# Optimization experiments

Hardware: AMD Instinct MI355X
Metric: run time of the kernel (lower is better)

## Reference

```python
import jax, jax.numpy as jnp
import numpy as np

NUM_HEADS = 8
AGENT_NUM = 144
POOL_SIZE = 12  # int(sqrt(agent_num))


def _adaptive_pool_matrix(H, out):
    # Row i averages input rows [floor(i*H/out), ceil((i+1)*H/out)) -- PyTorch AdaptiveAvgPool2d semantics.
    P = np.zeros((out, H), dtype=np.float32)
    for i in range(out):
        s = (i * H) // out
        e = -((-(i + 1) * H) // out)
        P[i, s:e] = 1.0 / (e - s)
    return jnp.asarray(P)


def setup_inputs() -> dict:
    key = jax.random.key(0)
    ks = jax.random.split(key, 4)
    b, n, c = 16, 3136, 512
    return {
        "x": jax.random.normal(ks[0], (b, n, c), dtype=jnp.float32),
        "qkv_w": jax.random.normal(ks[1], (3 * c, c), dtype=jnp.float32) * 0.02,
        "proj_w": jax.random.normal(ks[2], (c, c), dtype=jnp.float32) * 0.02,
        "proj_b": jnp.zeros((c,), dtype=jnp.float32),
        "dwc_w": jax.random.normal(ks[3], (c, 1, 3, 3), dtype=jnp.float32) * 0.1,
        "dwc_b": jnp.zeros((c,), dtype=jnp.float32),
    }


def reference(x, qkv_w, proj_w, proj_b, dwc_w, dwc_b):
    b, n, c = x.shape
    H = NUM_HEADS
    d = c // H
    hh = int(n ** 0.5)  # 56
    scale = d ** -0.5

    qkv = x @ qkv_w.T  # (b, n, 3c)
    q, k, v = jnp.split(qkv, 3, axis=-1)

    # adaptive avg pool of q (as b,h,w,c image) down to 12x12 -> agent tokens
    P = _adaptive_pool_matrix(hh, POOL_SIZE)  # (12, 56)
    agent = jnp.einsum('ph,qw,bhwc->bpqc', P, P, q.reshape(b, hh, hh, c))
    agent = agent.reshape(b, AGENT_NUM, c)

    def heads(t):
        return t.reshape(b, -1, H, d).transpose(0, 2, 1, 3)  # (b, H, L, d)

    qh, kh, vh, ah = heads(q), heads(k), heads(v), heads(agent)

    # stage 1: agent-to-key attention
    agent_attn = jax.nn.softmax((ah * scale) @ kh.transpose(0, 1, 3, 2), axis=-1)  # (b,H,144,n)
    agent_v = agent_attn @ vh  # (b,H,144,d)

    # stage 2: query-to-agent attention
    q_attn = jax.nn.softmax((qh * scale) @ ah.transpose(0, 1, 3, 2), axis=-1)  # (b,H,n,144)
    out = (q_attn @ agent_v).transpose(0, 2, 1, 3).reshape(b, n, c)

    # depthwise 3x3 conv residual on v image
    v_img = v.reshape(b, hh, hh, c).transpose(0, 3, 1, 2)  # NCHW
    dw = jax.lax.conv_general_dilated(
        v_img, dwc_w, window_strides=(1, 1), padding='SAME',
        feature_group_count=c, dimension_numbers=('NCHW', 'OIHW', 'NCHW'))
    dw = dw + dwc_b[None, :, None, None]
    out = out + dw.transpose(0, 2, 3, 1).reshape(b, n, c)

    return out @ proj_w.T + proj_b
```

## Files before the change

### kernel.cpp

```cpp
#include <hip/hip_runtime.h>
#include <hip/hip_bf16.h>
#include <math.h>

typedef unsigned short u16;
typedef __attribute__((ext_vector_type(8))) unsigned short u16x8;
typedef __attribute__((ext_vector_type(8))) short bf16x8;
typedef __attribute__((ext_vector_type(4))) float f32x4;

#define BATCH 16
#define NTOK  3136
#define CHN   512
#define NH    8
#define HD    64
#define HHW   56
#define NAG   144
#define PS    12

#define S1PP   72
#define S2PP   152
#define ASP    72
#define AVP    152
#define TRP    136

__device__ __forceinline__ float b2f(u16 u) {
    unsigned int x = ((unsigned int)u) << 16;
    float f;
    __builtin_memcpy(&f, &x, 4);
    return f;
}
__device__ __forceinline__ u16 f2b(float f) {
    unsigned int x;
    __builtin_memcpy(&x, &f, 4);
    unsigned int lsb = (x >> 16) & 1u;
    x += 0x7fffu + lsb;
    return (u16)(x >> 16);
}
__device__ __forceinline__ void store1(float* p, float v) { *p = v; }
__device__ __forceinline__ void store1(u16* p, float v)   { *p = f2b(v); }

__global__ __launch_bounds__(256) void cvt_f32_bf16_kernel(
    const float* __restrict__ src, u16* __restrict__ dst, int n4)
{
    const int idx = blockIdx.x * 256 + threadIdx.x;
    if (idx >= n4) return;
    float4 v = reinterpret_cast<const float4*>(src)[idx];
    ushort4 o;
    o.x = f2b(v.x); o.y = f2b(v.y); o.z = f2b(v.z); o.w = f2b(v.w);
    reinterpret_cast<ushort4*>(dst)[idx] = o;
}

template <typename OT, bool BIAS, bool TRB>
__global__ __launch_bounds__(256) void mfma_gemm_kernel(
    const u16* __restrict__ A, const u16* __restrict__ W,
    const float* __restrict__ bias, OT* __restrict__ out,
    u16* __restrict__ vt_out)
{
    __shared__ u16 SH[TRB ? 128 * TRP : 16384];
    u16* Asm = SH;
    u16* Bsm = SH + 8192;

    const int tid  = threadIdx.x;
    const int lane = tid & 63;
    const int w    = tid >> 6;

    const int nwg = gridDim.x * gridDim.y;
    const int lid = blockIdx.y * gridDim.x + blockIdx.x;
    int wid = lid;
    if ((nwg & 7) == 0) {
        const int chunk = nwg >> 3;
        wid = (lid & 7) * chunk + (lid >> 3);
    }
    const int m0 = (wid >> 2) * 128;
    const int n0 = (wid & 3) * 128;

    const int wm   = (w & 1) * 64;
    const int wn   = (w >> 1) * 64;

    const int srow = lane >> 3;
    const int scol = (lane & 7) * 8;

    f32x4 acc[4][4] = {};

    for (int kt = 0; kt < 8; ++kt) {
        const int k0 = kt * 64;
        __syncthreads();
        #pragma unroll
        for (int i = 0; i < 4; ++i) {
            const int rb = w * 8 + i * 32;
            __builtin_amdgcn_global_load_lds(
                (const __attribute__((address_space(1))) void*)
                    (A + (size_t)(m0 + rb + srow) * 512 + k0 + scol),
                (__attribute__((address_space(3))) void*)(Asm + rb * 64),
                16, 0, 0);
        }
        #pragma unroll
        for (int i = 0; i < 4; ++i) {
            const int rb = w * 8 + i * 32;
            __builtin_amdgcn_global_load_lds(
                (const __attribute__((address_space(1))) void*)
                    (W + (size_t)(n0 + rb + srow) * 512 + k0 + scol),
                (__attribute__((address_space(3))) void*)(Bsm + rb * 64),
                16, 0, 0);
        }
        __syncthreads();

        #pragma unroll
        for (int kh = 0; kh < 2; ++kh) {
            bf16x8 af[4], bfr[4];
            #pragma unroll
            for (int t = 0; t < 4; ++t)
                af[t] = *reinterpret_cast<const bf16x8*>(
                    &Asm[(wm + t * 16 + (lane & 15)) * 64 + kh * 32 + (lane >> 4) * 8]);
            #pragma unroll
            for (int t = 0; t < 4; ++t)
                bfr[t] = *reinterpret_cast<const bf16x8*>(
                    &Bsm[(wn + t * 16 + (lane & 15)) * 64 + kh * 32 + (lane >> 4) * 8]);
            #pragma unroll
            for (int i = 0; i < 4; ++i)
                #pragma unroll
                for (int j = 0; j < 4; ++j)
                    acc[i][j] = __builtin_amdgcn_mfma_f32_16x16x32_bf16(
                        af[i], bfr[j], acc[i][j], 0, 0, 0);
        }
    }

    const int quad = lane >> 4;
    const int col  = lane & 15;
    #pragma unroll
    for (int j = 0; j < 4; ++j) {
        const int n = n0 + wn + j * 16 + col;
        const float bv = BIAS ? bias[n] : 0.f;
        #pragma unroll
        for (int i = 0; i < 4; ++i) {
            #pragma unroll
            for (int r = 0; r < 4; ++r) {
                const int m = m0 + wm + i * 16 + quad * 4 + r;
                store1(&out[(size_t)m * 512 + n], acc[i][j][r] + bv);
            }
        }
    }

    if constexpr (TRB) {
        __syncthreads();
        #pragma unroll
        for (int j = 0; j < 4; ++j) {
            const int nl = wn + j * 16 + col;
            #pragma unroll
            for (int i = 0; i < 4; ++i)
                #pragma unroll
                for (int r = 0; r < 4; ++r) {
                    const int ml = wm + i * 16 + quad * 4 + r;
                    SH[nl * TRP + ml] = f2b(acc[i][j][r]);
                }
        }
        __syncthreads();
        const int nr = tid >> 1, mh = (tid & 1) * 64;
        const int ng = n0 + nr;
        #pragma unroll
        for (int kc = 0; kc < 8; ++kc) {
            const int ml  = mh + kc * 8;
            const int gm  = m0 + ml;
            const int bb  = gm / NTOK;
            const int tok = gm - bb * NTOK;
            u16x8 val = *reinterpret_cast<const u16x8*>(&SH[nr * TRP + ml]);
            *reinterpret_cast<u16x8*>(
                &vt_out[((size_t)bb * CHN + ng) * NTOK + tok]) = val;
        }
    }
}

__global__ __launch_bounds__(256) void pool_x_kernel(
    const float* __restrict__ x, u16* __restrict__ x_pool)
{
    const int b = blockIdx.x, pq = blockIdx.y;
    const int p = pq / PS, qq = pq % PS;
    const int sp_ = (p * HHW) / PS, ep_ = ((p + 1) * HHW + PS - 1) / PS;
    const int sq_ = (qq * HHW) / PS, eq_ = ((qq + 1) * HHW + PS - 1) / PS;
    const float inv = 1.0f / (float)((ep_ - sp_) * (eq_ - sq_));
    for (int ch = threadIdx.x; ch < CHN; ch += 256) {
        float acc = 0.f;
        for (int y = sp_; y < ep_; ++y)
            for (int xx = sq_; xx < eq_; ++xx)
                acc += x[((size_t)b * NTOK + y * HHW + xx) * CHN + ch];
        x_pool[((size_t)b * NAG + pq) * CHN + ch] = f2b(acc * inv);
    }
}

__global__ __launch_bounds__(64) void stage1_mfma_kernel(
    const u16* __restrict__ k, const u16* __restrict__ vt,
    const u16* __restrict__ agent, u16* __restrict__ avt)
{
    __shared__ u16 Pl[16 * S1PP];

    const int lb   = blockIdx.x;
    const int work = (lb & 7) * 144 + (lb >> 3);
    const int at   = work % 9;
    const int r2   = work / 9;
    const int h    = r2 & 7;
    const int b    = r2 >> 3;

    const int lane = threadIdx.x;
    const int c = lane & 15, g = lane >> 4;

    const u16* kp = k  + (size_t)b * NTOK * CHN + h * HD;
    const u16* vp = vt + ((size_t)(b * NH + h)) * HD * NTOK;
    const u16* ap = agent + ((size_t)b * NAG + at * 16 + c) * CHN + h * HD + g * 8;

    bf16x8 af0 = *reinterpret_cast<const bf16x8*>(ap);
    bf16x8 af1 = *reinterpret_cast<const bf16x8*>(ap + 32);

    f32x4 accO[4] = {};
    float m_ = -1e30f, l_ = 0.f;

    bf16x8 kf[8];
    #pragma unroll
    for (int kt = 0; kt < 4; ++kt)
        #pragma unroll
        for (int ks = 0; ks < 2; ++ks)
            kf[kt * 2 + ks] = *reinterpret_cast<const bf16x8*>(
                kp + (size_t)(kt * 16 + c) * CHN + ks * 32 + g * 8);

    for (int key0 = 0; key0 < NTOK; key0 += 64) {
        bf16x8 vf[8];
        #pragma unroll
        for (int dt = 0; dt < 4; ++dt)
            #pragma unroll
            for (int kk = 0; kk < 2; ++kk)
                vf[dt * 2 + kk] = *reinterpret_cast<const bf16x8*>(
                    vp + (size_t)(dt * 16 + c) * NTOK + key0 + kk * 32 + g * 8);
        bf16x8 kn[8];
        const bool more = (key0 + 64) < NTOK;
        if (more) {
            #pragma unroll
            for (int kt = 0; kt < 4; ++kt)
                #pragma unroll
                for (int ks = 0; ks < 2; ++ks)
                    kn[kt * 2 + ks] = *reinterpret_cast<const bf16x8*>(
                        kp + (size_t)(key0 + 64 + kt * 16 + c) * CHN + ks * 32 + g * 8);
        }

        f32x4 s[4] = {};
        #pragma unroll
        for (int kt = 0; kt < 4; ++kt) {
            s[kt] = __builtin_amdgcn_mfma_f32_16x16x32_bf16(kf[kt * 2 + 0], af0, s[kt], 0, 0, 0);
            s[kt] = __builtin_amdgcn_mfma_f32_16x16x32_bf16(kf[kt * 2 + 1], af1, s[kt], 0, 0, 0);
        }

        float tmax = -1e30f;
        #pragma unroll
        for (int kt = 0; kt < 4; ++kt)
            #pragma unroll
            for (int r = 0; r < 4; ++r) tmax = fmaxf(tmax, s[kt][r]);
        tmax = fmaxf(tmax, __shfl_xor(tmax, 16));
        tmax = fmaxf(tmax, __shfl_xor(tmax, 32));

        const float mnew  = fmaxf(m_, tmax * 0.125f);
        const float alpha = __expf(m_ - mnew);
        float psum = 0.f;
        #pragma unroll
        for (int kt = 0; kt < 4; ++kt) {
            float p0 = __expf(s[kt][0] * 0.125f - mnew);
            float p1 = __expf(s[kt][1] * 0.125f - mnew);
            float p2 = __expf(s[kt][2] * 0.125f - mnew);
            float p3 = __expf(s[kt][3] * 0.125f - mnew);
            psum += (p0 + p1) + (p2 + p3);
            ushort4 pk;
            pk.x = f2b(p0); pk.y = f2b(p1); pk.z = f2b(p2); pk.w = f2b(p3);
            *reinterpret_cast<ushort4*>(&Pl[c * S1PP + kt * 16 + g * 4]) = pk;
        }
        psum += __shfl_xor(psum, 16);
        psum += __shfl_xor(psum, 32);
        l_ = l_ * alpha + psum;
        m_ = mnew;
        #pragma unroll
        for (int dt = 0; dt < 4; ++dt) {
            accO[dt][0] *= alpha; accO[dt][1] *= alpha;
            accO[dt][2] *= alpha; accO[dt][3] *= alpha;
        }

        asm volatile("s_waitcnt lgkmcnt(0)" ::: "memory");
        __builtin_amdgcn_sched_barrier(0);

        bf16x8 pf0 = *reinterpret_cast<const bf16x8*>(&Pl[c * S1PP + g * 8]);
        bf16x8 pf1 = *reinterpret_cast<const bf16x8*>(&Pl[c * S1PP + 32 + g * 8]);

        #pragma unroll
        for (int dt = 0; dt < 4; ++dt) {
            accO[dt] = __builtin_amdgcn_mfma_f32_16x16x32_bf16(vf[dt * 2 + 0], pf0, accO[dt], 0, 0, 0);
            accO[dt] = __builtin_amdgcn_mfma_f32_16x16x32_bf16(vf[dt * 2 + 1], pf1, accO[dt], 0, 0, 0);
        }

        if (more) {
            #pragma unroll
            for (int i = 0; i < 8; ++i) kf[i] = kn[i];
        }
    }

    const float invl = 1.f / l_;
    const size_t dbase = (size_t)(b * NH + h) * HD;
    #pragma unroll
    for (int dt = 0; dt < 4; ++dt)
        #pragma unroll
        for (int r = 0; r < 4; ++r)
            avt[(dbase + dt * 16 + g * 4 + r) * NAG + at * 16 + c] =
                f2b(accO[dt][r] * invl);
}

__global__ __launch_bounds__(256, 3) void stage2_mfma_kernel(
    const u16* __restrict__ q,
    const u16* __restrict__ agent,
    const u16* __restrict__ avt,
    const u16* __restrict__ v,
    const float* __restrict__ dwc_w,
    const float* __restrict__ dwc_b,
    u16* __restrict__ xattn)
{
    __shared__ __align__(16) u16 AsPl[NAG * ASP];
    __shared__ __align__(16) u16 AVs[HD * AVP];
    __shared__ float dwW[HD * 9];
    __shared__ float dwB[HD];

    const int h   = blockIdx.y;
    const int b   = blockIdx.z;
    const int tid = threadIdx.x;
    const int w    = tid >> 6;
    const int lane = tid & 63;
    const int c = lane & 15, g = lane >> 4;
    const int q0 = (blockIdx.x * 4 + w) * 16;
    const int qg = q0 + c;
    const int y = qg / HHW, xx = qg % HHW;

    const u16* qp = q + ((size_t)b * NTOK + qg) * CHN + h * HD + g * 8;
    bf16x8 qf0 = *reinterpret_cast<const bf16x8*>(qp);
    bf16x8 qf1 = *reinterpret_cast<const bf16x8*>(qp + 32);

    {
        const u16* ab = agent + (size_t)b * NAG * CHN + h * HD;
        for (int idx = tid; idx < NAG * 4; idx += 256) {
            const int r = idx >> 2, cc = (idx & 3) * 16;
            *reinterpret_cast<u16x8*>(&AsPl[r * ASP + cc]) =
                *reinterpret_cast<const u16x8*>(ab + (size_t)r * CHN + cc);
            *reinterpret_cast<u16x8*>(&AsPl[r * ASP + cc + 8]) =
                *reinterpret_cast<const u16x8*>(ab + (size_t)r * CHN + cc + 8);
        }
        const u16* avb = avt + (size_t)(b * NH + h) * HD * NAG;
        for (int idx = tid; idx < HD * 18; idx += 256) {
            const int r = idx / 18, cc = (idx % 18) * 8;
            *reinterpret_cast<u16x8*>(&AVs[r * AVP + cc]) =
                *reinterpret_cast<const u16x8*>(avb + (size_t)r * NAG + cc);
        }
        for (int idx = tid; idx < HD * 9; idx += 256)
            dwW[idx] = dwc_w[(h * HD + idx / 9) * 9 + (idx % 9)];
        if (tid < HD) dwB[tid] = dwc_b[h * HD + tid];
    }
    __syncthreads();

    float conv[4][4];
    #pragma unroll
    for (int dt = 0; dt < 4; ++dt)
        #pragma unroll
        for (int r = 0; r < 4; ++r) conv[dt][r] = 0.f;
    {
        const u16* vq = v + ((size_t)b * NTOK + qg) * CHN + h * HD + g * 4;
        #pragma unroll
        for (int dy = -1; dy <= 1; ++dy) {
            #pragma unroll
            for (int dx = -1; dx <= 1; ++dx) {
                const int tap = (dy + 1) * 3 + (dx + 1);
                const int yy = y + dy, xc = xx + dx;
                const bool ok = (yy >= 0 && yy < HHW && xc >= 0 && xc < HHW);
                const u16* vr = vq + (ok ? (ptrdiff_t)(dy * HHW + dx) * CHN : 0);
                ushort4 vv0 = *reinterpret_cast<const ushort4*>(vr);
                ushort4 vv1 = *reinterpret_cast<const ushort4*>(vr + 16);
                ushort4 vv2 = *reinterpret_cast<const ushort4*>(vr + 32);
                ushort4 vv3 = *reinterpret_cast<const ushort4*>(vr + 48);
                if (ok) {
                    const float* wt = &dwW[(g * 4) * 9 + tap];
                    conv[0][0] += b2f(vv0.x) * wt[(0 * 16 + 0) * 9];
                    conv[0][1] += b2f(vv0.y) * wt[(0 * 16 + 1) * 9];
                    conv[0][2] += b2f(vv0.z) * wt[(0 * 16 + 2) * 9];
                    conv[0][3] += b2f(vv0.w) * wt[(0 * 16 + 3) * 9];
                    conv[1][0] += b2f(vv1.x) * wt[(1 * 16 + 0) * 9];
                    conv[1][1] += b2f(vv1.y) * wt[(1 * 16 + 1) * 9];
                    conv[1][2] += b2f(vv1.z) * wt[(1 * 16 + 2) * 9];
                    conv[1][3] += b2f(vv1.w) * wt[(1 * 16 + 3) * 9];
                    conv[2][0] += b2f(vv2.x) * wt[(2 * 16 + 0) * 9];
                    conv[2][1] += b2f(vv2.y) * wt[(2 * 16 + 1) * 9];
                    conv[2][2] += b2f(vv2.z) * wt[(2 * 16 + 2) * 9];
                    conv[2][3] += b2f(vv2.w) * wt[(2 * 16 + 3) * 9];
                    conv[3][0] += b2f(vv3.x) * wt[(3 * 16 + 0) * 9];
                    conv[3][1] += b2f(vv3.y) * wt[(3 * 16 + 1) * 9];
                    conv[3][2] += b2f(vv3.z) * wt[(3 * 16 + 2) * 9];
                    conv[3][3] += b2f(vv3.w) * wt[(3 * 16 + 3) * 9];
                }
            }
        }
    }

    f32x4 s[9] = {};
    #pragma unroll
    for (int t = 0; t < 9; ++t) {
        bf16x8 af0 = *reinterpret_cast<const bf16x8*>(&AsPl[(t * 16 + c) * ASP + g * 8]);
        bf16x8 af1 = *reinterpret_cast<const bf16x8*>(&AsPl[(t * 16 + c) * ASP + 32 + g * 8]);
        s[t] = __builtin_amdgcn_mfma_f32_16x16x32_bf16(af0, qf0, s[t], 0, 0, 0);
        s[t] = __builtin_amdgcn_mfma_f32_16x16x32_bf16(af1, qf1, s[t], 0, 0, 0);
    }

    __syncthreads();

    float mx = -1e30f;
    #pragma unroll
    for (int t = 0; t < 9; ++t)
        #pragma unroll
        for (int r = 0; r < 4; ++r) mx = fmaxf(mx, s[t][r]);
    mx = fmaxf(mx, __shfl_xor(mx, 16));
    mx = fmaxf(mx, __shfl_xor(mx, 32));
    mx *= 0.125f;

    u16* Pw = &AsPl[w * 16 * S2PP];
    float ls = 0.f;
    #pragma unroll
    for (int t = 0; t < 9; ++t) {
        float p0 = __expf(s[t][0] * 0.125f - mx);
        float p1 = __expf(s[t][1] * 0.125f - mx);
        float p2 = __expf(s[t][2] * 0.125f - mx);
        float p3 = __expf(s[t][3] * 0.125f - mx);
        ls += (p0 + p1) + (p2 + p3);
        ushort4 pk;
        pk.x = f2b(p0); pk.y = f2b(p1); pk.z = f2b(p2); pk.w = f2b(p3);
        *reinterpret_cast<ushort4*>(&Pw[c * S2PP + t * 16 + g * 4]) = pk;
    }
    ls += __shfl_xor(ls, 16);
    ls += __shfl_xor(ls, 32);
    const float inv = 1.f / ls;

    asm volatile("s_waitcnt lgkmcnt(0)" ::: "memory");
    __builtin_amdgcn_sched_barrier(0);

    f32x4 o[4] = {};
    #pragma unroll
    for (int sl = 0; sl < 4; ++sl) {
        bf16x8 pf = *reinterpret_cast<const bf16x8*>(&Pw[c * S2PP + sl * 32 + g * 8]);
        #pragma unroll
        for (int dt = 0; dt < 4; ++dt) {
            bf16x8 avf = *reinterpret_cast<const bf16x8*>(
                &AVs[(dt * 16 + c) * AVP + sl * 32 + g * 8]);
            o[dt] = __builtin_amdgcn_mfma_f32_16x16x32_bf16(avf, pf, o[dt], 0, 0, 0);
        }
    }
    {
        bf16x8 pf = {};
        bf16x8 avf[4] = {{0,0,0,0,0,0,0,0},{0,0,0,0,0,0,0,0},
                         {0,0,0,0,0,0,0,0},{0,0,0,0,0,0,0,0}};
        if (g < 2) {
            pf = *reinterpret_cast<const bf16x8*>(&Pw[c * S2PP + 128 + g * 8]);
            #pragma unroll
            for (int dt = 0; dt < 4; ++dt)
                avf[dt] = *reinterpret_cast<const bf16x8*>(
                    &AVs[(dt * 16 + c) * AVP + 128 + g * 8]);
        }
        #pragma unroll
        for (int dt = 0; dt < 4; ++dt)
            o[dt] = __builtin_amdgcn_mfma_f32_16x16x32_bf16(avf[dt], pf, o[dt], 0, 0, 0);
    }

    u16* outp = xattn + ((size_t)b * NTOK + qg) * CHN + h * HD + g * 4;
    #pragma unroll
    for (int dt = 0; dt < 4; ++dt) {
        ushort4 o4;
        o4.x = f2b(o[dt][0] * inv + dwB[dt * 16 + g * 4 + 0] + conv[dt][0]);
        o4.y = f2b(o[dt][1] * inv + dwB[dt * 16 + g * 4 + 1] + conv[dt][1]);
        o4.z = f2b(o[dt][2] * inv + dwB[dt * 16 + g * 4 + 2] + conv[dt][2]);
        o4.w = f2b(o[dt][3] * inv + dwB[dt * 16 + g * 4 + 3] + conv[dt][3]);
        *reinterpret_cast<ushort4*>(outp + dt * 16) = o4;
    }
}

extern "C" void kernel_launch(void* const* d_in, const int* in_sizes, int n_in,
                              void* d_out, int out_size, void* d_ws, size_t ws_size,
                              hipStream_t stream)
{
    const float* x      = (const float*)d_in[0];
    const float* qkv_w  = (const float*)d_in[1];
    const float* proj_w = (const float*)d_in[2];
    const float* proj_b = (const float*)d_in[3];
    const float* dwc_w  = (const float*)d_in[4];
    const float* dwc_b  = (const float*)d_in[5];
    float* out = (float*)d_out;

    const size_t nqkv = (size_t)BATCH * NTOK * CHN;
    u16* xb  = (u16*)d_out;
    u16* vt  = xb + nqkv;
    u16* qb  = xb + nqkv;
    u16* kb  = (u16*)d_in[0];
    u16* vb  = kb + nqkv;
    u16* attn = kb;

    char* p = (char*)d_ws;
    u16* x_pool  = (u16*)p;  p += (size_t)BATCH * NAG * CHN * 2;
    u16* agent   = (u16*)p;  p += (size_t)BATCH * NAG * CHN * 2;
    u16* avt     = (u16*)p;  p += (size_t)BATCH * NH * HD * NAG * 2;
    u16* wb      = (u16*)p;
    u16* Wq_b = wb;
    u16* Wk_b = wb + (size_t)262144;
    u16* Wv_b = wb + (size_t)524288;
    u16* Wp_b = wb + (size_t)786432;

    pool_x_kernel<<<dim3(BATCH, NAG), 256, 0, stream>>>(x, x_pool);
    cvt_f32_bf16_kernel<<<(int)(nqkv / 4 + 255) / 256, 256, 0, stream>>>(x, xb, (int)(nqkv / 4));
    cvt_f32_bf16_kernel<<<(786432 / 4 + 255) / 256, 256, 0, stream>>>(qkv_w, wb, 786432 / 4);
    cvt_f32_bf16_kernel<<<(262144 / 4 + 255) / 256, 256, 0, stream>>>(proj_w, Wp_b, 262144 / 4);
    mfma_gemm_kernel<u16, false, false><<<dim3(18, 4), 256, 0, stream>>>(
        x_pool, Wq_b, nullptr, agent, nullptr);
    mfma_gemm_kernel<u16, false, false><<<dim3(392, 4), 256, 0, stream>>>(
        xb, Wk_b, nullptr, kb, nullptr);
    mfma_gemm_kernel<u16, false, true><<<dim3(392, 4), 256, 0, stream>>>(
        xb, Wv_b, nullptr, vb, vt);
    stage1_mfma_kernel<<<dim3(1152), 64, 0, stream>>>(kb, vt, agent, avt);
    mfma_gemm_kernel<u16, false, false><<<dim3(392, 4), 256, 0, stream>>>(
        xb, Wq_b, nullptr, qb, nullptr);
    stage2_mfma_kernel<<<dim3(49, NH, BATCH), 256, 0, stream>>>(
        qb, agent, avt, vb, dwc_w, dwc_b, attn);
    mfma_gemm_kernel<float, true, false><<<dim3(392, 4), 256, 0, stream>>>(
        attn, Wp_b, proj_b, out, nullptr);
}
```

Before: 711.4 us.

## Split stage-1 key loop across four waves with flash-decoding style merge

The stage-1 agent-to-key attention kernel now runs four wavefronts per block. Each wave processes a contiguous slice of the 49 key tiles with its own online-softmax state. The partial maxima, sums and outputs are then merged through shared memory by wave 0. This shortens the serial key loop per block and raises parallelism from 1152 single-wave blocks, in exchange for extra LDS traffic and a final reduction step.

```diff
diff --git a/kernel.cpp b/kernel.cpp
--- a/kernel.cpp
+++ b/kernel.cpp
@@ -186,11 +186,13 @@
     }
 }
 
-__global__ __launch_bounds__(64) void stage1_mfma_kernel(
+__global__ __launch_bounds__(256) void stage1_mfma_kernel(
     const u16* __restrict__ k, const u16* __restrict__ vt,
     const u16* __restrict__ agent, u16* __restrict__ avt)
 {
-    __shared__ u16 Pl[16 * S1PP];
+    __shared__ u16   Pl[4][16 * S1PP];
+    __shared__ float Mg[4][16], Lg[4][16];
+    __shared__ float Og[4][64][17];
 
     const int lb   = blockIdx.x;
     const int work = (lb & 7) * 144 + (lb >> 3);
@@ -199,8 +201,13 @@
     const int h    = r2 & 7;
     const int b    = r2 >> 3;
 
-    const int lane = threadIdx.x;
+    const int tid  = threadIdx.x;
+    const int w    = tid >> 6;
+    const int lane = tid & 63;
     const int c = lane & 15, g = lane >> 4;
+
+    const int tstart = (w == 0) ? 0 : (13 + (w - 1) * 12);
+    const int tend   = tstart + ((w == 0) ? 13 : 12);
 
     const u16* kp = k  + (size_t)b * NTOK * CHN + h * HD;
     const u16* vp = vt + ((size_t)(b * NH + h)) * HD * NTOK;
@@ -212,15 +219,18 @@
     f32x4 accO[4] = {};
     float m_ = -1e30f, l_ = 0.f;
 
+    u16* Plw = Pl[w];
+
     bf16x8 kf[8];
     #pragma unroll
     for (int kt = 0; kt < 4; ++kt)
         #pragma unroll
         for (int ks = 0; ks < 2; ++ks)
             kf[kt * 2 + ks] = *reinterpret_cast<const bf16x8*>(
-                kp + (size_t)(kt * 16 + c) * CHN + ks * 32 + g * 8);
-
-    for (int key0 = 0; key0 < NTOK; key0 += 64) {
+                kp + (size_t)(tstart * 64 + kt * 16 + c) * CHN + ks * 32 + g * 8);
+
+    for (int t = tstart; t < tend; ++t) {
+        const int key0 = t * 64;
         bf16x8 vf[8];
         #pragma unroll
         for (int dt = 0; dt < 4; ++dt)
@@ -229,7 +239,7 @@
                 vf[dt * 2 + kk] = *reinterpret_cast<const bf16x8*>(
                     vp + (size_t)(dt * 16 + c) * NTOK + key0 + kk * 32 + g * 8);
         bf16x8 kn[8];
-        const bool more = (key0 + 64) < NTOK;
+        const bool more = (t + 1) < tend;
         if (more) {
             #pragma unroll
             for (int kt = 0; kt < 4; ++kt)
@@ -266,7 +276,7 @@
             psum += (p0 + p1) + (p2 + p3);
             ushort4 pk;
             pk.x = f2b(p0); pk.y = f2b(p1); pk.z = f2b(p2); pk.w = f2b(p3);
-            *reinterpret_cast<ushort4*>(&Pl[c * S1PP + kt * 16 + g * 4]) = pk;
+            *reinterpret_cast<ushort4*>(&Plw[c * S1PP + kt * 16 + g * 4]) = pk;
         }
         psum += __shfl_xor(psum, 16);
         psum += __shfl_xor(psum, 32);
@@ -281,8 +291,8 @@
         asm volatile("s_waitcnt lgkmcnt(0)" ::: "memory");
         __builtin_amdgcn_sched_barrier(0);
 
-        bf16x8 pf0 = *reinterpret_cast<const bf16x8*>(&Pl[c * S1PP + g * 8]);
-        bf16x8 pf1 = *reinterpret_cast<const bf16x8*>(&Pl[c * S1PP + 32 + g * 8]);
+        bf16x8 pf0 = *reinterpret_cast<const bf16x8*>(&Plw[c * S1PP + g * 8]);
+        bf16x8 pf1 = *reinterpret_cast<const bf16x8*>(&Plw[c * S1PP + 32 + g * 8]);
 
         #pragma unroll
         for (int dt = 0; dt < 4; ++dt) {
@@ -296,14 +306,34 @@
         }
     }
 
-    const float invl = 1.f / l_;
-    const size_t dbase = (size_t)(b * NH + h) * HD;
+    if (g == 0) { Mg[w][c] = m_; Lg[w][c] = l_; }
     #pragma unroll
     for (int dt = 0; dt < 4; ++dt)
         #pragma unroll
         for (int r = 0; r < 4; ++r)
-            avt[(dbase + dt * 16 + g * 4 + r) * NAG + at * 16 + c] =
-                f2b(accO[dt][r] * invl);
+            Og[w][lane][dt * 4 + r] = accO[dt][r];
+    __syncthreads();
+
+    if (w == 0) {
+        const float m0_ = Mg[0][c], m1_ = Mg[1][c], m2_ = Mg[2][c], m3_ = Mg[3][c];
+        const float ms  = fmaxf(fmaxf(m0_, m1_), fmaxf(m2_, m3_));
+        const float s0 = __expf(m0_ - ms), s1 = __expf(m1_ - ms),
+                    s2 = __expf(m2_ - ms), s3 = __expf(m3_ - ms);
+        const float ls = Lg[0][c] * s0 + Lg[1][c] * s1 +
+                         Lg[2][c] * s2 + Lg[3][c] * s3;
+        const float invl = 1.f / ls;
+        const size_t dbase = (size_t)(b * NH + h) * HD;
+        #pragma unroll
+        for (int dt = 0; dt < 4; ++dt)
+            #pragma unroll
+            for (int r = 0; r < 4; ++r) {
+                const int i = dt * 4 + r;
+                const float val = Og[0][lane][i] * s0 + Og[1][lane][i] * s1 +
+                                  Og[2][lane][i] * s2 + Og[3][lane][i] * s3;
+                avt[(dbase + dt * 16 + g * 4 + r) * NAG + at * 16 + c] =
+                    f2b(val * invl);
+            }
+    }
 }
 
 __global__ __launch_bounds__(256, 3) void stage2_mfma_kernel(
@@ -516,7 +546,7 @@
         xb, Wk_b, nullptr, kb, nullptr);
     mfma_gemm_kernel<u16, false, true><<<dim3(392, 4), 256, 0, stream>>>(
         xb, Wv_b, nullptr, vb, vt);
-    stage1_mfma_kernel<<<dim3(1152), 64, 0, stream>>>(kb, vt, agent, avt);
+    stage1_mfma_kernel<<<dim3(1152), 256, 0, stream>>>(kb, vt, agent, avt);
     mfma_gemm_kernel<u16, false, false><<<dim3(392, 4), 256, 0, stream>>>(
         xb, Wq_b, nullptr, qb, nullptr);
     stage2_mfma_kernel<<<dim3(49, NH, BATCH), 256, 0, stream>>>(
```

Measured after the change: 707.7 us. No clear change (-0.5%).
